# Performance work log

Hardware: AMD Instinct MI355X
Metric: run time of the kernel (lower is better)

Reference implementation:

```python
import jax, jax.numpy as jnp
import numpy as np
from jax import lax

N_NEURONS = 2500
K = 50
T = 60
F = 5
H = 128
GROUP_SIZES = [800, 700, 600, 400]  # support_resistance, trend, pattern, volume
GID = jnp.asarray(np.repeat(np.arange(4), GROUP_SIZES))  # [N] specialty id per neuron
_BOUNDS = np.cumsum([0] + GROUP_SIZES)


def _lstm_layer(x, w_ih, w_hh, b_ih, b_hh):
    # x: [B,T,in]; PyTorch gate order i,f,g,o in the 4H weight rows
    B = x.shape[0]
    Hd = w_hh.shape[1]
    def step(carry, xt):
        h, c = carry
        g = xt @ w_ih.T + h @ w_hh.T + b_ih + b_hh
        i, f, gg, o = jnp.split(g, 4, axis=-1)
        c = jax.nn.sigmoid(f) * c + jax.nn.sigmoid(i) * jnp.tanh(gg)
        h = jax.nn.sigmoid(o) * jnp.tanh(c)
        return (h, c), h
    init = (jnp.zeros((B, Hd), x.dtype), jnp.zeros((B, Hd), x.dtype))
    (h, _), ys = lax.scan(step, init, jnp.swapaxes(x, 0, 1))
    return jnp.swapaxes(ys, 0, 1), h


def _forward(x, w_ih0, w_hh0, b_ih0, b_hh0, w_ih1, w_hh1, b_ih1, b_hh1,
             pw1, pb1, pw2, pb2, conn_w, sens, thr,
             iw1, ib1, iw2, ib2, iw3, ib3,
             hw_trend, hb_trend, hw_pat, hb_pat, hw_key, hb_key,
             hw_vol, hb_vol, hw_conf, hb_conf, conn_idx):
    seq, _ = _lstm_layer(x, w_ih0, w_hh0, b_ih0, b_hh0)
    _, h2 = _lstm_layer(seq, w_ih1, w_hh1, b_ih1, b_hh1)  # hidden[-1]: [B,H]
    # feature_projection: Linear->ReLU->Linear->Tanh
    base = jnp.tanh(jax.nn.relu(h2 @ pw1.T + pb1) @ pw2.T + pb2)  # [B,32]
    # broadcast base features to a per-neuron activation vector [B,N]
    reps = -(-N_NEURONS // base.shape[1])
    all_act = jnp.tile(base, (1, reps))[:, :N_NEURONS]
    # batched sparse gather + per-neuron weighted sum
    gathered = all_act[:, conn_idx]                       # [B,N,K]
    z = jnp.einsum('bnk,nk->bn', gathered, conn_w) * sens  # [B,N]
    # specialty-conditioned activation
    a = jnp.where(GID == 0, jax.nn.sigmoid(z - thr),
        jnp.where(GID == 1, jnp.tanh(z),
        jnp.where(GID == 2, jax.nn.relu(z - thr), jax.nn.sigmoid(z))))
    # integrator (dropout is eval-mode no-op)
    integ = jnp.tanh(jax.nn.relu(jax.nn.relu(a @ iw1.T + ib1) @ iw2.T + ib2) @ iw3.T + ib3)
    trend = integ @ hw_trend.T + hb_trend      # [B,3]
    pat = integ @ hw_pat.T + hb_pat            # [B,6]
    key_l = integ @ hw_key.T + hb_key          # [B,4]
    vol = integ @ hw_vol.T + hb_vol            # [B,1]
    conf = integ @ hw_conf.T + hb_conf         # [B,1]
    overall = jax.nn.sigmoid(conf)             # [B,1]
    means = jnp.stack([a[:, _BOUNDS[i]:_BOUNDS[i + 1]].mean(axis=1) for i in range(4)], axis=1)
    return jnp.concatenate([trend, pat, key_l, vol, conf, overall, means], axis=1)  # [B,20]


def setup_inputs() -> dict:
    key = jax.random.key(0)
    ks = iter(jax.random.split(key, 64))
    def rn(shape, s=0.05):
        return jax.random.normal(next(ks), shape, jnp.float32) * s
    B = 1024
    return {
        'x': jax.random.normal(next(ks), (B, T, F), jnp.float32),
        'conn_idx': jax.random.randint(next(ks), (N_NEURONS, K), 0, N_NEURONS, jnp.int32),
        'w_ih0': rn((4 * H, F)), 'w_hh0': rn((4 * H, H)),
        'b_ih0': rn((4 * H,), 0.01), 'b_hh0': rn((4 * H,), 0.01),
        'w_ih1': rn((4 * H, H)), 'w_hh1': rn((4 * H, H)),
        'b_ih1': rn((4 * H,), 0.01), 'b_hh1': rn((4 * H,), 0.01),
        'pw1': rn((64, H)), 'pb1': rn((64,), 0.01),
        'pw2': rn((32, 64)), 'pb2': rn((32,), 0.01),
        'conn_w': rn((N_NEURONS, K), 0.1),
        'sens': rn((N_NEURONS,), 0.1) + 1.0,
        'thr': rn((N_NEURONS,), 0.1) + 0.6,
        'iw1': rn((256, N_NEURONS), 0.01), 'ib1': rn((256,), 0.01),
        'iw2': rn((64, 256)), 'ib2': rn((64,), 0.01),
        'iw3': rn((32, 64)), 'ib3': rn((32,), 0.01),
        'hw_trend': rn((3, 32)), 'hb_trend': rn((3,), 0.01),
        'hw_pat': rn((6, 32)), 'hb_pat': rn((6,), 0.01),
        'hw_key': rn((4, 32)), 'hb_key': rn((4,), 0.01),
        'hw_vol': rn((1, 32)), 'hb_vol': rn((1,), 0.01),
        'hw_conf': rn((1, 32)), 'hb_conf': rn((1,), 0.01),
    }


def reference(x, conn_idx, w_ih0, w_hh0, b_ih0, b_hh0, w_ih1, w_hh1, b_ih1, b_hh1,
              pw1, pb1, pw2, pb2, conn_w, sens, thr,
              iw1, ib1, iw2, ib2, iw3, ib3,
              hw_trend, hb_trend, hw_pat, hb_pat, hw_key, hb_key,
              hw_vol, hb_vol, hw_conf, hb_conf):
    return _forward(x, w_ih0, w_hh0, b_ih0, b_hh0, w_ih1, w_hh1, b_ih1, b_hh1,
                    pw1, pb1, pw2, pb2, conn_w, sens, thr,
                    iw1, ib1, iw2, ib2, iw3, ib3,
                    hw_trend, hb_trend, hw_pat, hb_pat, hw_key, hb_key,
                    hw_vol, hb_vol, hw_conf, hb_conf, conn_idx)
```

## Files before the change

kernel.cpp:

```cpp
#include <hip/hip_runtime.h>
#include <hip/hip_bf16.h>
#include <math.h>

#define DEV __device__ __forceinline__

typedef short short8 __attribute__((ext_vector_type(8)));
typedef float f32x4  __attribute__((ext_vector_type(4)));

DEV float sigf(float x)   { return 1.0f / (1.0f + __expf(-x)); }
DEV float tanhft(float x) { return 1.0f - 2.0f / (__expf(2.0f * x) + 1.0f); }

DEV unsigned short f2bf(float f) {
    unsigned int u = __float_as_uint(f);
    unsigned int r = (u + 0x7FFFu + ((u >> 16) & 1u)) >> 16;
    return (unsigned short)r;
}
DEV float bf2f(unsigned short u) {
    return __uint_as_float(((unsigned int)u) << 16);
}

DEV void bar_lds() {
    asm volatile("s_waitcnt lgkmcnt(0)" ::: "memory");
    __builtin_amdgcn_s_barrier();
}

__global__ __launch_bounds__(256) void prep_all_kernel(
    const float* __restrict__ w_hh0, const float* __restrict__ w_ih1,
    const float* __restrict__ w_hh1,
    const float* __restrict__ b_ih0, const float* __restrict__ b_hh0,
    const float* __restrict__ b_ih1, const float* __restrict__ b_hh1,
    const int* __restrict__ conn_idx, const float* __restrict__ conn_w,
    const float* __restrict__ iw1,
    unsigned short* __restrict__ whh0h, unsigned short* __restrict__ wih1h,
    unsigned short* __restrict__ whh1h,
    float* __restrict__ bias0, float* __restrict__ bias1,
    float* __restrict__ weffT, unsigned short* __restrict__ iw1b)
{
    __shared__ float s[128 * 33];
    const int blk = blockIdx.x;
    if (blk < 258) {
        int i = blk * 256 + threadIdx.x;
        if (i < 65536) {
            whh0h[i] = f2bf(w_hh0[i]);
            wih1h[i] = f2bf(w_ih1[i]);
            whh1h[i] = f2bf(w_hh1[i]);
        } else if (i < 66048) {
            int c = i - 65536;
            bias0[c] = b_ih0[c] + b_hh0[c];
            bias1[c] = b_ih1[c] + b_hh1[c];
        }
    } else if (blk < 278) {
        int tid = threadIdx.x;
        if (tid < 128) {
            int n = (blk - 258) * 128 + tid;
            float* sr = &s[tid * 33];
#pragma unroll
            for (int j = 0; j < 32; ++j) sr[j] = 0.f;
            if (n < 2500) {
                for (int k = 0; k < 50; ++k) {
                    int idx = conn_idx[n * 50 + k];
                    sr[idx & 31] += conn_w[n * 50 + k];
                }
                for (int j = 0; j < 32; ++j) weffT[j * 2500 + n] = sr[j];
            }
        }
    } else {
        int i = (blk - 278) * 256 + threadIdx.x;
        if (i < 256 * 2528) {
            int row = i / 2528, k = i - row * 2528;
            iw1b[i] = (k < 2500) ? f2bf(iw1[row * 2500 + k]) : (unsigned short)0;
        }
    }
}

__global__ __launch_bounds__(512, 2) void lstm_kernel(
    const float* __restrict__ x,
    const unsigned short* __restrict__ whh0,
    const unsigned short* __restrict__ wih1,
    const unsigned short* __restrict__ whh1,
    const float* __restrict__ wih0,
    const float* __restrict__ bias0, const float* __restrict__ bias1,
    float* __restrict__ h2out)
{
    __shared__ __align__(16) float          xs[4][304];
    __shared__ __align__(16) unsigned short h0s[2][16][136];
    __shared__ __align__(16) unsigned short h1s[2][16][136];
    __shared__ __align__(16) float          wsc[8][4][16][4];
    __shared__ float wih0s[2560];

    const int tid = threadIdx.x;
    const int b0  = blockIdx.x * 4;
    const int l15 = tid & 15;
    const int q   = (tid >> 4) & 3;
    const int w   = tid >> 6;
    const int j   = w * 16 + l15;
    const int q8  = q * 8;

    for (int i = tid; i < 1200; i += 512) {
        int m = i / 300, kk = i - m * 300;
        xs[m][kk] = x[(b0 + m) * 300 + kk];
    }
    for (int i = tid; i < 2560; i += 512) wih0s[i] = wih0[i];
    for (int i = tid; i < 2176; i += 512) {
        ((unsigned int*)h0s)[i] = 0u;
        ((unsigned int*)h1s)[i] = 0u;
    }

    float ub0[4], ub1[4];
#pragma unroll
    for (int g = 0; g < 4; ++g) {
        ub0[g] = bias0[g * 128 + j];
        ub1[g] = bias1[g * 128 + j];
    }

    short8 bh0[4][4], b1i[4][4];
#pragma unroll
    for (int g = 0; g < 4; ++g)
#pragma unroll
        for (int kc = 0; kc < 4; ++kc) {
            int off = (g * 128 + j) * 128 + kc * 32 + q8;
            bh0[g][kc] = *(const short8*)(whh0 + off);
            b1i[g][kc] = *(const short8*)(wih1 + off);
        }

    float c0 = 0.f, c1 = 0.f, hl = 0.f;
    __syncthreads();

    const unsigned short* wsb = whh1 + j * 128 + q8;

    for (int t = 0; t < 60; ++t) {
        const int p = t & 1;

        short8 wsv[4][4];
#pragma unroll
        for (int g = 0; g < 4; ++g) {
            wsv[g][0] = *(const short8*)(wsb + g * 16384);
            wsv[g][1] = *(const short8*)(wsb + g * 16384 + 32);
        }

        f32x4 acc[4];
#pragma unroll
        for (int g = 0; g < 4; ++g) acc[g] = (f32x4){0.f, 0.f, 0.f, 0.f};
        short8 af[4];
#pragma unroll
        for (int kc = 0; kc < 4; ++kc)
            af[kc] = *(const short8*)&h0s[p][l15][kc * 32 + q8];
#pragma unroll
        for (int kc = 0; kc < 4; ++kc)
#pragma unroll
            for (int g = 0; g < 4; ++g)
                acc[g] = __builtin_amdgcn_mfma_f32_16x16x32_bf16(af[kc], bh0[g][kc], acc[g], 0, 0, 0);

#pragma unroll
        for (int g = 0; g < 4; ++g) {
            wsv[g][2] = *(const short8*)(wsb + g * 16384 + 64);
            wsv[g][3] = *(const short8*)(wsb + g * 16384 + 96);
        }

        if (q == 0) {
#pragma unroll
            for (int g = 0; g < 4; ++g)
                *(f32x4*)&wsc[w][g][l15][0] = acc[g];
        }
        {
            const float* xr = &xs[q][t * 5];
            float x0 = xr[0], x1 = xr[1], x2 = xr[2], x3 = xr[3], x4 = xr[4];
            float gv[4];
#pragma unroll
            for (int g = 0; g < 4; ++g) {
                const float* wr = &wih0s[(g * 128 + j) * 5];
                float s = wsc[w][g][l15][q] + ub0[g];
                s = fmaf(x0, wr[0], s);
                s = fmaf(x1, wr[1], s);
                s = fmaf(x2, wr[2], s);
                s = fmaf(x3, wr[3], s);
                gv[g] = fmaf(x4, wr[4], s);
            }
            c0 = sigf(gv[1]) * c0 + sigf(gv[0]) * tanhft(gv[2]);
            float h = sigf(gv[3]) * tanhft(c0);
            h0s[1 - p][q][j] = f2bf(h);
        }

        bar_lds();

#pragma unroll
        for (int g = 0; g < 4; ++g) acc[g] = (f32x4){0.f, 0.f, 0.f, 0.f};
#pragma unroll
        for (int kc = 0; kc < 4; ++kc)
            af[kc] = *(const short8*)&h0s[1 - p][l15][kc * 32 + q8];
#pragma unroll
        for (int kc = 0; kc < 4; ++kc)
#pragma unroll
            for (int g = 0; g < 4; ++g)
                acc[g] = __builtin_amdgcn_mfma_f32_16x16x32_bf16(af[kc], b1i[g][kc], acc[g], 0, 0, 0);
#pragma unroll
        for (int kc = 0; kc < 4; ++kc)
            af[kc] = *(const short8*)&h1s[p][l15][kc * 32 + q8];
#pragma unroll
        for (int kc = 0; kc < 4; ++kc)
#pragma unroll
            for (int g = 0; g < 4; ++g)
                acc[g] = __builtin_amdgcn_mfma_f32_16x16x32_bf16(af[kc], wsv[g][kc], acc[g], 0, 0, 0);

        if (q == 0) {
#pragma unroll
            for (int g = 0; g < 4; ++g)
                *(f32x4*)&wsc[w][g][l15][0] = acc[g];
        }
        {
            float gv[4];
#pragma unroll
            for (int g = 0; g < 4; ++g)
                gv[g] = wsc[w][g][l15][q] + ub1[g];
            c1 = sigf(gv[1]) * c1 + sigf(gv[0]) * tanhft(gv[2]);
            float h = sigf(gv[3]) * tanhft(c1);
            h1s[1 - p][q][j] = f2bf(h);
            hl = h;
        }
    }

    h2out[(b0 + q) * 128 + j] = hl;
}

__global__ __launch_bounds__(256) void phase2_kernel(
    const float* __restrict__ h2, const float* __restrict__ pw1,
    const float* __restrict__ pb1, const float* __restrict__ pw2,
    const float* __restrict__ pb2, float* __restrict__ base)
{
    __shared__ float pw1s[64 * 129];
    __shared__ float pw2s[32 * 65];
    __shared__ float hs[4][128];
    __shared__ float p1s[4][64];

    const int tid = threadIdx.x;
    const int b0  = blockIdx.x * 4;

    for (int i = tid; i < 8192; i += 256) {
        int u = i >> 7, k = i & 127;
        pw1s[u * 129 + k] = pw1[i];
    }
    for (int i = tid; i < 2048; i += 256) {
        int u = i >> 6, k = i & 63;
        pw2s[u * 65 + k] = pw2[i];
    }
    for (int i = tid; i < 512; i += 256)
        hs[i >> 7][i & 127] = h2[b0 * 128 + i];
    __syncthreads();

    {
        const int r = tid >> 6, u = tid & 63;
        float acc = pb1[u];
        const float* wr = &pw1s[u * 129];
        const float* hr = &hs[r][0];
#pragma unroll 4
        for (int k = 0; k < 128; ++k) acc = fmaf(hr[k], wr[k], acc);
        p1s[r][u] = fmaxf(acc, 0.f);
    }
    __syncthreads();

    if (tid < 128) {
        const int r = tid >> 5, u2 = tid & 31;
        float a2 = pb2[u2];
        const float* wr = &pw2s[u2 * 65];
        const float* pr = &p1s[r][0];
#pragma unroll 4
        for (int k = 0; k < 64; ++k) a2 = fmaf(pr[k], wr[k], a2);
        base[(b0 + r) * 32 + u2] = tanhft(a2);
    }
}

__global__ __launch_bounds__(256) void za_kernel(
    const float* __restrict__ base, const float* __restrict__ weffT,
    const float* __restrict__ sens, const float* __restrict__ thr,
    unsigned short* __restrict__ amat)
{
    __shared__ float bs[16][32];
    int tid = threadIdx.x;
    int bb = blockIdx.x / 10, nb = blockIdx.x % 10;
    int n = nb * 256 + tid;
    bool nv = n < 2500;
    bool pv = n < 2528;
    int nn = nv ? n : 0;
    for (int i = tid; i < 512; i += 256) bs[i >> 5][i & 31] = base[bb * 512 + i];
    __syncthreads();
    float w[32];
#pragma unroll
    for (int j = 0; j < 32; ++j) w[j] = weffT[j * 2500 + nn];
    float sn = sens[nn], tn = thr[nn];
    int g = (n < 800) ? 0 : (n < 1500) ? 1 : (n < 2100) ? 2 : 3;
#pragma unroll 2
    for (int r = 0; r < 16; ++r) {
        float z = 0.f;
#pragma unroll
        for (int j = 0; j < 32; ++j) z = fmaf(bs[r][j], w[j], z);
        z *= sn;
        float av;
        if (g == 0)      av = sigf(z - tn);
        else if (g == 1) av = tanhft(z);
        else if (g == 2) av = fmaxf(z - tn, 0.f);
        else             av = sigf(z);
        if (nv)      amat[(bb * 16 + r) * 2528 + n] = f2bf(av);
        else if (pv) amat[(bb * 16 + r) * 2528 + n] = 0;
    }
}

__global__ __launch_bounds__(128) void gemm_iw1_kernel(
    const unsigned short* __restrict__ ab, const unsigned short* __restrict__ wb,
    const float* __restrict__ ib1, float* __restrict__ t1)
{
    const int tid = threadIdx.x;
    const int wv  = tid >> 6;
    const int l15 = tid & 15, q = (tid >> 4) & 3, q8 = q * 8;
    const int row0 = blockIdx.y * 32 + wv * 16;
    const int col0 = blockIdx.x * 32;

    const unsigned short* A = ab + (row0 + l15) * 2528 + q8;
    const unsigned short* B = wb + (col0 + l15) * 2528 + q8;

    short8 a = *(const short8*)A;
    short8 b[2];
#pragma unroll
    for (int nt = 0; nt < 2; ++nt) b[nt] = *(const short8*)(B + nt * 16 * 2528);

    f32x4 acc[2];
#pragma unroll
    for (int nt = 0; nt < 2; ++nt) acc[nt] = (f32x4){0.f, 0.f, 0.f, 0.f};

    for (int c = 0; c < 79; ++c) {
        int cn = (c < 78) ? c + 1 : 78;
        short8 an = *(const short8*)(A + cn * 32);
        short8 bn[2];
#pragma unroll
        for (int nt = 0; nt < 2; ++nt)
            bn[nt] = *(const short8*)(B + nt * 16 * 2528 + cn * 32);
#pragma unroll
        for (int nt = 0; nt < 2; ++nt)
            acc[nt] = __builtin_amdgcn_mfma_f32_16x16x32_bf16(a, b[nt], acc[nt], 0, 0, 0);
        a = an;
#pragma unroll
        for (int nt = 0; nt < 2; ++nt) b[nt] = bn[nt];
    }

#pragma unroll
    for (int nt = 0; nt < 2; ++nt) {
        int n = col0 + nt * 16 + l15;
        float bias = ib1[n];
#pragma unroll
        for (int i = 0; i < 4; ++i) {
            int row = row0 + q * 4 + i;
            t1[row * 256 + n] = fmaxf(acc[nt][i] + bias, 0.f);
        }
    }
}

__global__ __launch_bounds__(256) void final_kernel(
    const float* __restrict__ t1, const unsigned short* __restrict__ amat,
    const float* __restrict__ iw2,
    const float* __restrict__ ib2, const float* __restrict__ iw3,
    const float* __restrict__ ib3,
    const float* __restrict__ hw_trend, const float* __restrict__ hb_trend,
    const float* __restrict__ hw_pat,   const float* __restrict__ hb_pat,
    const float* __restrict__ hw_key,   const float* __restrict__ hb_key,
    const float* __restrict__ hw_vol,   const float* __restrict__ hb_vol,
    const float* __restrict__ hw_conf,  const float* __restrict__ hb_conf,
    float* __restrict__ out)
{
    __shared__ float iw2s[64 * 257];
    __shared__ float iw3s[32 * 65];
    __shared__ float t1s[4][256];
    __shared__ float t2s[4][64];
    __shared__ float igs[4][32];
    __shared__ float mred[4][4];

    const int tid = threadIdx.x;
    const int b0  = blockIdx.x * 4;

    for (int i = tid; i < 16384; i += 256) {
        int u = i >> 8, k = i & 255;
        iw2s[u * 257 + k] = iw2[i];
    }
    for (int i = tid; i < 2048; i += 256) {
        int u = i >> 6, k = i & 63;
        iw3s[u * 65 + k] = iw3[i];
    }
    for (int i = tid; i < 1024; i += 256)
        t1s[i >> 8][i & 255] = t1[b0 * 256 + i];

    {
        const int lane = tid & 63, wv4 = tid >> 6;
        const unsigned short* arow = amat + (unsigned int)(b0 + wv4) * 2528;
        float parts[4] = {0.f, 0.f, 0.f, 0.f};
#pragma unroll
        for (int s = 0; s < 5; ++s) {
            int c = lane + 64 * s;
            if (c < 316) {
                short8 v = *(const short8*)(arow + c * 8);
#pragma unroll
                for (int e = 0; e < 8; ++e) {
                    int n = c * 8 + e;
                    float f = bf2f((unsigned short)v[e]);
                    if (n < 800)       parts[0] += f;
                    else if (n < 1500) parts[1] += f;
                    else if (n < 2100) parts[2] += f;
                    else               parts[3] += f;
                }
            }
        }
#pragma unroll
        for (int g = 0; g < 4; ++g) {
            float v = parts[g];
            for (int s2 = 32; s2 > 0; s2 >>= 1) v += __shfl_down(v, s2, 64);
            if (lane == 0) mred[wv4][g] = v;
        }
    }
    __syncthreads();

    {
        const int r = tid >> 6, u = tid & 63;
        float acc = ib2[u];
        const float* wr = &iw2s[u * 257];
        const float* tr = &t1s[r][0];
#pragma unroll 4
        for (int k = 0; k < 256; ++k) acc = fmaf(tr[k], wr[k], acc);
        t2s[r][u] = fmaxf(acc, 0.f);
    }
    __syncthreads();

    if (tid < 128) {
        const int r = tid >> 5, u2 = tid & 31;
        float a2 = ib3[u2];
        const float* wr = &iw3s[u2 * 65];
        const float* tr = &t2s[r][0];
#pragma unroll 4
        for (int k = 0; k < 64; ++k) a2 = fmaf(tr[k], wr[k], a2);
        igs[r][u2] = tanhft(a2);
    }
    __syncthreads();

    if (tid < 60) {
        const int r = tid / 15, t15 = tid % 15;
        const int b = b0 + r;
        const float* w; const float* bb; int j, off;
        if (t15 < 3)        { w = hw_trend; bb = hb_trend; j = t15;     off = 0; }
        else if (t15 < 9)   { w = hw_pat;   bb = hb_pat;   j = t15 - 3; off = 3; }
        else if (t15 < 13)  { w = hw_key;   bb = hb_key;   j = t15 - 9; off = 9; }
        else if (t15 == 13) { w = hw_vol;   bb = hb_vol;   j = 0;       off = 13; }
        else                { w = hw_conf;  bb = hb_conf;  j = 0;       off = 14; }
        float a3 = bb[j];
#pragma unroll
        for (int k = 0; k < 32; ++k) a3 = fmaf(igs[r][k], w[j * 32 + k], a3);
        out[b * 20 + off + j] = a3;
        if (t15 == 14) out[b * 20 + 15] = sigf(a3);
    }
    if (tid < 16) {
        const int r = tid >> 2, g = tid & 3;
        const float inv[4] = {1.f / 800.f, 1.f / 700.f, 1.f / 600.f, 1.f / 400.f};
        out[(b0 + r) * 20 + 16 + g] = mred[r][g] * inv[g];
    }
}

extern "C" void kernel_launch(void* const* d_in, const int* in_sizes, int n_in,
                              void* d_out, int out_size, void* d_ws, size_t ws_size,
                              hipStream_t stream)
{
    const float* x        = (const float*)d_in[0];
    const int*   conn_idx = (const int*)  d_in[1];
    const float* w_ih0    = (const float*)d_in[2];
    const float* w_hh0    = (const float*)d_in[3];
    const float* b_ih0    = (const float*)d_in[4];
    const float* b_hh0    = (const float*)d_in[5];
    const float* w_ih1    = (const float*)d_in[6];
    const float* w_hh1    = (const float*)d_in[7];
    const float* b_ih1    = (const float*)d_in[8];
    const float* b_hh1    = (const float*)d_in[9];
    const float* pw1      = (const float*)d_in[10];
    const float* pb1      = (const float*)d_in[11];
    const float* pw2      = (const float*)d_in[12];
    const float* pb2      = (const float*)d_in[13];
    const float* conn_w   = (const float*)d_in[14];
    const float* sens     = (const float*)d_in[15];
    const float* thr      = (const float*)d_in[16];
    const float* iw1      = (const float*)d_in[17];
    const float* ib1      = (const float*)d_in[18];
    const float* iw2      = (const float*)d_in[19];
    const float* ib2      = (const float*)d_in[20];
    const float* iw3      = (const float*)d_in[21];
    const float* ib3      = (const float*)d_in[22];
    const float* hw_trend = (const float*)d_in[23];
    const float* hb_trend = (const float*)d_in[24];
    const float* hw_pat   = (const float*)d_in[25];
    const float* hb_pat   = (const float*)d_in[26];
    const float* hw_key   = (const float*)d_in[27];
    const float* hb_key   = (const float*)d_in[28];
    const float* hw_vol   = (const float*)d_in[29];
    const float* hb_vol   = (const float*)d_in[30];
    const float* hw_conf  = (const float*)d_in[31];
    const float* hb_conf  = (const float*)d_in[32];
    float* out = (float*)d_out;
    float* ws  = (float*)d_ws;

    unsigned short* whh0h = (unsigned short*)(ws);
    unsigned short* wih1h = (unsigned short*)(ws + 32768);
    unsigned short* whh1h = (unsigned short*)(ws + 65536);
    float* bias0  = ws + 98304;
    float* bias1  = ws + 98816;
    float* h2     = ws + 99328;
    float* base_  = ws + 230400;
    float* weffT  = ws + 263168;
    float* t1     = ws + 343168;
    unsigned short* iw1b   = (unsigned short*)(ws + 605312);
    unsigned short* amatbf = (unsigned short*)(ws + 928896);

    prep_all_kernel<<<2806, 256, 0, stream>>>(w_hh0, w_ih1, w_hh1,
                                              b_ih0, b_hh0, b_ih1, b_hh1,
                                              conn_idx, conn_w, iw1,
                                              whh0h, wih1h, whh1h, bias0, bias1,
                                              weffT, iw1b);
    lstm_kernel<<<256, 512, 0, stream>>>(x, whh0h, wih1h, whh1h, w_ih0,
                                         bias0, bias1, h2);
    phase2_kernel<<<256, 256, 0, stream>>>(h2, pw1, pb1, pw2, pb2, base_);
    za_kernel<<<640, 256, 0, stream>>>(base_, weffT, sens, thr, amatbf);
    gemm_iw1_kernel<<<dim3(8, 32), 128, 0, stream>>>(amatbf, iw1b, ib1, t1);
    final_kernel<<<256, 256, 0, stream>>>(t1, amatbf, iw2, ib2, iw3, ib3,
                                          hw_trend, hb_trend, hw_pat, hb_pat,
                                          hw_key, hb_key, hw_vol, hb_vol,
                                          hw_conf, hb_conf, out);
}
```

Before: 286.5 us.

## Fuse projection, neuron activation, iw1 GEMM and heads into one tail kernel

Merges phase2, za, gemm_iw1 and final kernels into a single 512-thread kernel per 4-row batch tile, keeping base features, the bf16 activation matrix and t1 in shared memory. This removes three launches and the global round trips for the intermediates. In exchange, each block recomputes weffT loads and streams the whole iw1 matrix with MFMA tiles that use only 4 of 16 rows. It also carries large LDS use (about 140KB), which limits occupancy.

```diff
diff --git a/kernel.cpp b/kernel.cpp
--- a/kernel.cpp
+++ b/kernel.cpp
@@ -222,32 +222,51 @@
     h2out[(b0 + q) * 128 + j] = hl;
 }
 
-__global__ __launch_bounds__(256) void phase2_kernel(
-    const float* __restrict__ h2, const float* __restrict__ pw1,
-    const float* __restrict__ pb1, const float* __restrict__ pw2,
-    const float* __restrict__ pb2, float* __restrict__ base)
+__global__ __launch_bounds__(512) void tail_kernel(
+    const float* __restrict__ h2,
+    const float* __restrict__ pw1, const float* __restrict__ pb1,
+    const float* __restrict__ pw2, const float* __restrict__ pb2,
+    const float* __restrict__ weffT,
+    const float* __restrict__ sens, const float* __restrict__ thr,
+    const unsigned short* __restrict__ iw1b, const float* __restrict__ ib1,
+    const float* __restrict__ iw2, const float* __restrict__ ib2,
+    const float* __restrict__ iw3, const float* __restrict__ ib3,
+    const float* __restrict__ hw_trend, const float* __restrict__ hb_trend,
+    const float* __restrict__ hw_pat,   const float* __restrict__ hb_pat,
+    const float* __restrict__ hw_key,   const float* __restrict__ hb_key,
+    const float* __restrict__ hw_vol,   const float* __restrict__ hb_vol,
+    const float* __restrict__ hw_conf,  const float* __restrict__ hb_conf,
+    float* __restrict__ out)
 {
     __shared__ float pw1s[64 * 129];
     __shared__ float pw2s[32 * 65];
     __shared__ float hs[4][128];
     __shared__ float p1s[4][64];
+    __shared__ float base_s[4][32];
+    __shared__ __align__(16) unsigned short amat_s[4][2528];
+    __shared__ float t1s[4][256];
+    __shared__ float iw2s[64 * 257];
+    __shared__ float iw3s[32 * 65];
+    __shared__ float t2s[4][64];
+    __shared__ float igs[4][32];
+    __shared__ float mred[4][4];
 
     const int tid = threadIdx.x;
     const int b0  = blockIdx.x * 4;
 
-    for (int i = tid; i < 8192; i += 256) {
-        int u = i >> 7, k = i & 127;
-        pw1s[u * 129 + k] = pw1[i];
-    }
-    for (int i = tid; i < 2048; i += 256) {
-        int u = i >> 6, k = i & 63;
-        pw2s[u * 65 + k] = pw2[i];
-    }
-    for (int i = tid; i < 512; i += 256)
+    for (int i = tid; i < 8192; i += 512)
+        pw1s[(i >> 7) * 129 + (i & 127)] = pw1[i];
+    for (int i = tid; i < 2048; i += 512)
+        pw2s[(i >> 6) * 65 + (i & 63)] = pw2[i];
+    for (int i = tid; i < 16384; i += 512)
+        iw2s[(i >> 8) * 257 + (i & 255)] = iw2[i];
+    for (int i = tid; i < 2048; i += 512)
+        iw3s[(i >> 6) * 65 + (i & 63)] = iw3[i];
+    for (int i = tid; i < 512; i += 512)
         hs[i >> 7][i & 127] = h2[b0 * 128 + i];
     __syncthreads();
 
-    {
+    if (tid < 256) {
         const int r = tid >> 6, u = tid & 63;
         float acc = pb1[u];
         const float* wr = &pw1s[u * 129];
@@ -257,7 +276,6 @@
         p1s[r][u] = fmaxf(acc, 0.f);
     }
     __syncthreads();
-
     if (tid < 128) {
         const int r = tid >> 5, u2 = tid & 31;
         float a2 = pb2[u2];
@@ -265,136 +283,45 @@
         const float* pr = &p1s[r][0];
 #pragma unroll 4
         for (int k = 0; k < 64; ++k) a2 = fmaf(pr[k], wr[k], a2);
-        base[(b0 + r) * 32 + u2] = tanhft(a2);
-    }
-}
-
-__global__ __launch_bounds__(256) void za_kernel(
-    const float* __restrict__ base, const float* __restrict__ weffT,
-    const float* __restrict__ sens, const float* __restrict__ thr,
-    unsigned short* __restrict__ amat)
-{
-    __shared__ float bs[16][32];
-    int tid = threadIdx.x;
-    int bb = blockIdx.x / 10, nb = blockIdx.x % 10;
-    int n = nb * 256 + tid;
-    bool nv = n < 2500;
-    bool pv = n < 2528;
-    int nn = nv ? n : 0;
-    for (int i = tid; i < 512; i += 256) bs[i >> 5][i & 31] = base[bb * 512 + i];
-    __syncthreads();
-    float w[32];
-#pragma unroll
-    for (int j = 0; j < 32; ++j) w[j] = weffT[j * 2500 + nn];
-    float sn = sens[nn], tn = thr[nn];
-    int g = (n < 800) ? 0 : (n < 1500) ? 1 : (n < 2100) ? 2 : 3;
-#pragma unroll 2
-    for (int r = 0; r < 16; ++r) {
-        float z = 0.f;
-#pragma unroll
-        for (int j = 0; j < 32; ++j) z = fmaf(bs[r][j], w[j], z);
-        z *= sn;
-        float av;
-        if (g == 0)      av = sigf(z - tn);
-        else if (g == 1) av = tanhft(z);
-        else if (g == 2) av = fmaxf(z - tn, 0.f);
-        else             av = sigf(z);
-        if (nv)      amat[(bb * 16 + r) * 2528 + n] = f2bf(av);
-        else if (pv) amat[(bb * 16 + r) * 2528 + n] = 0;
-    }
-}
-
-__global__ __launch_bounds__(128) void gemm_iw1_kernel(
-    const unsigned short* __restrict__ ab, const unsigned short* __restrict__ wb,
-    const float* __restrict__ ib1, float* __restrict__ t1)
-{
-    const int tid = threadIdx.x;
-    const int wv  = tid >> 6;
-    const int l15 = tid & 15, q = (tid >> 4) & 3, q8 = q * 8;
-    const int row0 = blockIdx.y * 32 + wv * 16;
-    const int col0 = blockIdx.x * 32;
-
-    const unsigned short* A = ab + (row0 + l15) * 2528 + q8;
-    const unsigned short* B = wb + (col0 + l15) * 2528 + q8;
-
-    short8 a = *(const short8*)A;
-    short8 b[2];
-#pragma unroll
-    for (int nt = 0; nt < 2; ++nt) b[nt] = *(const short8*)(B + nt * 16 * 2528);
-
-    f32x4 acc[2];
-#pragma unroll
-    for (int nt = 0; nt < 2; ++nt) acc[nt] = (f32x4){0.f, 0.f, 0.f, 0.f};
-
-    for (int c = 0; c < 79; ++c) {
-        int cn = (c < 78) ? c + 1 : 78;
-        short8 an = *(const short8*)(A + cn * 32);
-        short8 bn[2];
-#pragma unroll
-        for (int nt = 0; nt < 2; ++nt)
-            bn[nt] = *(const short8*)(B + nt * 16 * 2528 + cn * 32);
-#pragma unroll
-        for (int nt = 0; nt < 2; ++nt)
-            acc[nt] = __builtin_amdgcn_mfma_f32_16x16x32_bf16(a, b[nt], acc[nt], 0, 0, 0);
-        a = an;
-#pragma unroll
-        for (int nt = 0; nt < 2; ++nt) b[nt] = bn[nt];
-    }
-
-#pragma unroll
-    for (int nt = 0; nt < 2; ++nt) {
-        int n = col0 + nt * 16 + l15;
-        float bias = ib1[n];
-#pragma unroll
-        for (int i = 0; i < 4; ++i) {
-            int row = row0 + q * 4 + i;
-            t1[row * 256 + n] = fmaxf(acc[nt][i] + bias, 0.f);
-        }
-    }
-}
-
-__global__ __launch_bounds__(256) void final_kernel(
-    const float* __restrict__ t1, const unsigned short* __restrict__ amat,
-    const float* __restrict__ iw2,
-    const float* __restrict__ ib2, const float* __restrict__ iw3,
-    const float* __restrict__ ib3,
-    const float* __restrict__ hw_trend, const float* __restrict__ hb_trend,
-    const float* __restrict__ hw_pat,   const float* __restrict__ hb_pat,
-    const float* __restrict__ hw_key,   const float* __restrict__ hb_key,
-    const float* __restrict__ hw_vol,   const float* __restrict__ hb_vol,
-    const float* __restrict__ hw_conf,  const float* __restrict__ hb_conf,
-    float* __restrict__ out)
-{
-    __shared__ float iw2s[64 * 257];
-    __shared__ float iw3s[32 * 65];
-    __shared__ float t1s[4][256];
-    __shared__ float t2s[4][64];
-    __shared__ float igs[4][32];
-    __shared__ float mred[4][4];
-
-    const int tid = threadIdx.x;
-    const int b0  = blockIdx.x * 4;
-
-    for (int i = tid; i < 16384; i += 256) {
-        int u = i >> 8, k = i & 255;
-        iw2s[u * 257 + k] = iw2[i];
-    }
-    for (int i = tid; i < 2048; i += 256) {
-        int u = i >> 6, k = i & 63;
-        iw3s[u * 65 + k] = iw3[i];
-    }
-    for (int i = tid; i < 1024; i += 256)
-        t1s[i >> 8][i & 255] = t1[b0 * 256 + i];
-
-    {
+        base_s[r][u2] = tanhft(a2);
+    }
+    __syncthreads();
+
+    for (int it = 0; it < 5; ++it) {
+        int n = it * 512 + tid;
+        if (n < 2528) {
+            bool nv = n < 2500;
+            int nn = nv ? n : 0;
+            float w[32];
+#pragma unroll
+            for (int j = 0; j < 32; ++j) w[j] = weffT[j * 2500 + nn];
+            float sn = sens[nn], tn = thr[nn];
+            int g = (n < 800) ? 0 : (n < 1500) ? 1 : (n < 2100) ? 2 : 3;
+#pragma unroll
+            for (int r = 0; r < 4; ++r) {
+                float z = 0.f;
+#pragma unroll
+                for (int j = 0; j < 32; ++j) z = fmaf(base_s[r][j], w[j], z);
+                z *= sn;
+                float av;
+                if (g == 0)      av = sigf(z - tn);
+                else if (g == 1) av = tanhft(z);
+                else if (g == 2) av = fmaxf(z - tn, 0.f);
+                else             av = sigf(z);
+                amat_s[r][n] = nv ? f2bf(av) : (unsigned short)0;
+            }
+        }
+    }
+    __syncthreads();
+
+    if (tid < 256) {
         const int lane = tid & 63, wv4 = tid >> 6;
-        const unsigned short* arow = amat + (unsigned int)(b0 + wv4) * 2528;
         float parts[4] = {0.f, 0.f, 0.f, 0.f};
 #pragma unroll
         for (int s = 0; s < 5; ++s) {
             int c = lane + 64 * s;
             if (c < 316) {
-                short8 v = *(const short8*)(arow + c * 8);
+                short8 v = *(const short8*)&amat_s[wv4][c * 8];
 #pragma unroll
                 for (int e = 0; e < 8; ++e) {
                     int n = c * 8 + e;
@@ -413,9 +340,54 @@
             if (lane == 0) mred[wv4][g] = v;
         }
     }
-    __syncthreads();
 
     {
+        const int wv  = tid >> 6;
+        const int l15 = tid & 15, qq = (tid >> 4) & 3, q8 = qq * 8;
+        const int col0 = wv * 32;
+
+        const unsigned short* B = iw1b + (col0 + l15) * 2528 + q8;
+
+        short8 a = (short8){0, 0, 0, 0, 0, 0, 0, 0};
+        if (l15 < 4) a = *(const short8*)&amat_s[l15][q8];
+        short8 b[2];
+#pragma unroll
+        for (int nt = 0; nt < 2; ++nt) b[nt] = *(const short8*)(B + nt * 16 * 2528);
+
+        f32x4 acc[2];
+#pragma unroll
+        for (int nt = 0; nt < 2; ++nt) acc[nt] = (f32x4){0.f, 0.f, 0.f, 0.f};
+
+        for (int c = 0; c < 79; ++c) {
+            int cn = (c < 78) ? c + 1 : 78;
+            short8 an = (short8){0, 0, 0, 0, 0, 0, 0, 0};
+            if (l15 < 4) an = *(const short8*)&amat_s[l15][cn * 32 + q8];
+            short8 bn[2];
+#pragma unroll
+            for (int nt = 0; nt < 2; ++nt)
+                bn[nt] = *(const short8*)(B + nt * 16 * 2528 + cn * 32);
+#pragma unroll
+            for (int nt = 0; nt < 2; ++nt)
+                acc[nt] = __builtin_amdgcn_mfma_f32_16x16x32_bf16(a, b[nt], acc[nt], 0, 0, 0);
+            a = an;
+#pragma unroll
+            for (int nt = 0; nt < 2; ++nt) b[nt] = bn[nt];
+        }
+
+        if (qq == 0) {
+#pragma unroll
+            for (int nt = 0; nt < 2; ++nt) {
+                int n = col0 + nt * 16 + l15;
+                float bias = ib1[n];
+#pragma unroll
+                for (int i = 0; i < 4; ++i)
+                    t1s[i][n] = fmaxf(acc[nt][i] + bias, 0.f);
+            }
+        }
+    }
+    __syncthreads();
+
+    if (tid < 256) {
         const int r = tid >> 6, u = tid & 63;
         float acc = ib2[u];
         const float* wr = &iw2s[u * 257];
@@ -425,7 +397,6 @@
         t2s[r][u] = fmaxf(acc, 0.f);
     }
     __syncthreads();
-
     if (tid < 128) {
         const int r = tid >> 5, u2 = tid & 31;
         float a2 = ib3[u2];
@@ -436,7 +407,6 @@
         igs[r][u2] = tanhft(a2);
     }
     __syncthreads();
-
     if (tid < 60) {
         const int r = tid / 15, t15 = tid % 15;
         const int b = b0 + r;
@@ -505,11 +475,8 @@
     float* bias0  = ws + 98304;
     float* bias1  = ws + 98816;
     float* h2     = ws + 99328;
-    float* base_  = ws + 230400;
     float* weffT  = ws + 263168;
-    float* t1     = ws + 343168;
-    unsigned short* iw1b   = (unsigned short*)(ws + 605312);
-    unsigned short* amatbf = (unsigned short*)(ws + 928896);
+    unsigned short* iw1b  = (unsigned short*)(ws + 605312);
 
     prep_all_kernel<<<2806, 256, 0, stream>>>(w_hh0, w_ih1, w_hh1,
                                               b_ih0, b_hh0, b_ih1, b_hh1,
@@ -518,11 +485,10 @@
                                               weffT, iw1b);
     lstm_kernel<<<256, 512, 0, stream>>>(x, whh0h, wih1h, whh1h, w_ih0,
                                          bias0, bias1, h2);
-    phase2_kernel<<<256, 256, 0, stream>>>(h2, pw1, pb1, pw2, pb2, base_);
-    za_kernel<<<640, 256, 0, stream>>>(base_, weffT, sens, thr, amatbf);
-    gemm_iw1_kernel<<<dim3(8, 32), 128, 0, stream>>>(amatbf, iw1b, ib1, t1);
-    final_kernel<<<256, 256, 0, stream>>>(t1, amatbf, iw2, ib2, iw3, ib3,
-                                          hw_trend, hb_trend, hw_pat, hb_pat,
-                                          hw_key, hb_key, hw_vol, hb_vol,
-                                          hw_conf, hb_conf, out);
-}
+    tail_kernel<<<256, 512, 0, stream>>>(h2, pw1, pb1, pw2, pb2,
+                                         weffT, sens, thr, iw1b, ib1,
+                                         iw2, ib2, iw3, ib3,
+                                         hw_trend, hb_trend, hw_pat, hb_pat,
+                                         hw_key, hb_key, hw_vol, hb_vol,
+                                         hw_conf, hb_conf, out);
+}
```

Result: slower. 294.0 us (+2.6%).
